# Performance work log

Hardware: AMD Instinct MI355X
Metric: run time of the kernel (lower is better)

Reference implementation:

```python
import jax, jax.numpy as jnp
import numpy as np

D_MODEL = 1024
NUM_HEADS = 16
D_K = D_MODEL // NUM_HEADS


def setup_inputs() -> dict:
    key = jax.random.key(0)
    ks = jax.random.split(key, 11)
    s = 1.0 / np.sqrt(D_MODEL)
    inp = {
        "Q": jax.random.normal(ks[0], (2, 2048, D_MODEL), jnp.float32),
        "K": jax.random.normal(ks[1], (2, 2048, D_MODEL), jnp.float32),
        "V": jax.random.normal(ks[2], (2, 2048, D_MODEL), jnp.float32),
        "W_q": jax.random.uniform(ks[3], (D_MODEL, D_MODEL), jnp.float32, -s, s),
        "b_q": jax.random.uniform(ks[4], (D_MODEL,), jnp.float32, -s, s),
        "W_k": jax.random.uniform(ks[5], (D_MODEL, D_MODEL), jnp.float32, -s, s),
        "b_k": jax.random.uniform(ks[6], (D_MODEL,), jnp.float32, -s, s),
        "W_v": jax.random.uniform(ks[7], (D_MODEL, D_MODEL), jnp.float32, -s, s),
        "b_v": jax.random.uniform(ks[8], (D_MODEL,), jnp.float32, -s, s),
        "W_o": jax.random.uniform(ks[9], (D_MODEL, D_MODEL), jnp.float32, -s, s),
        "b_o": jax.random.uniform(ks[10], (D_MODEL,), jnp.float32, -s, s),
    }
    return inp


def reference(Q, K, V, W_q, b_q, W_k, b_k, W_v, b_v, W_o, b_o):
    B, S, _ = Q.shape
    # Linear projections (torch Linear: x @ W.T + b; W here stored as [in, out])
    q = Q @ W_q + b_q
    k = K @ W_k + b_k
    v = V @ W_v + b_v
    # split heads -> [B, H, S, d_k]
    q = q.reshape(B, S, NUM_HEADS, D_K).transpose(0, 2, 1, 3)
    k = k.reshape(B, S, NUM_HEADS, D_K).transpose(0, 2, 1, 3)
    v = v.reshape(B, S, NUM_HEADS, D_K).transpose(0, 2, 1, 3)
    scale = 1.0 / np.sqrt(D_K).astype(np.float32)
    scores = jnp.einsum('bhqd,bhkd->bhqk', q, k) * scale  # [B,H,S,S]
    probs = jax.nn.softmax(scores, axis=-1)
    attn = jnp.einsum('bhqk,bhkd->bhqd', probs, v)  # [B,H,S,d_k]
    attn = attn.transpose(0, 2, 1, 3).reshape(B, S, D_MODEL)
    return attn @ W_o + b_o
```

## Files before the change

kernel.cpp:

```cpp
#include <hip/hip_runtime.h>
#include <math.h>

#define SEQ   2048
#define DM    1024
#define NH    16
#define DK    64
#define MTOT  4096
#define QSCALE 0.18033688011112043f

typedef __bf16 bf16x8 __attribute__((ext_vector_type(8)));
typedef float  f32x4  __attribute__((ext_vector_type(4)));
typedef unsigned short u16;
typedef unsigned long long u64;

__device__ __forceinline__ u16 f2bf(float f) {
    unsigned int u = __float_as_uint(f);
    u += 0x7fff + ((u >> 16) & 1);
    return (u16)(u >> 16);
}

__device__ __forceinline__ void async16(const void* g, void* l) {
    __builtin_amdgcn_global_load_lds(
        (const __attribute__((address_space(1))) unsigned int*)(unsigned long long)g,
        (__attribute__((address_space(3))) unsigned int*)(unsigned int)(unsigned long long)l,
        16, 0, 0);
}

__device__ __forceinline__ bf16x8 ld16(const u16* p) {
    bf16x8 v;
    __builtin_memcpy(&v, p, 16);
    return v;
}
__device__ __forceinline__ bf16x8 ld8x2(const u16* p) {
    union { u64 q[2]; bf16x8 v; } u;
    __builtin_memcpy(&u.q[0], p, 8);
    __builtin_memcpy(&u.q[1], p + 4, 8);
    return u.v;
}
__device__ __forceinline__ void st8(u16* p, unsigned int lo, unsigned int hi) {
    u64 q = ((u64)hi << 32) | lo;
    __builtin_memcpy(p, &q, 8);
}

__global__ __launch_bounds__(256)
void cvt_in(const float* __restrict__ Q, const float* __restrict__ K,
            const float* __restrict__ V, u16* __restrict__ Qb,
            u16* __restrict__ Kb, u16* __restrict__ Vb)
{
    const float* src; u16* dst;
    if (blockIdx.z == 0)      { src = Q; dst = Qb; }
    else if (blockIdx.z == 1) { src = K; dst = Kb; }
    else                      { src = V; dst = Vb; }
    const size_t i = ((size_t)blockIdx.x * 256 + threadIdx.x) * 8;
    float4 a = *(const float4*)&src[i];
    float4 b = *(const float4*)&src[i + 4];
    uint4 o;
    o.x = (unsigned)f2bf(a.x) | ((unsigned)f2bf(a.y) << 16);
    o.y = (unsigned)f2bf(a.z) | ((unsigned)f2bf(a.w) << 16);
    o.z = (unsigned)f2bf(b.x) | ((unsigned)f2bf(b.y) << 16);
    o.w = (unsigned)f2bf(b.z) | ((unsigned)f2bf(b.w) << 16);
    *(uint4*)&dst[i] = o;
}

__global__ __launch_bounds__(256)
void cvt_wt(const float* __restrict__ Wq, const float* __restrict__ Wk,
            const float* __restrict__ Wv, const float* __restrict__ Wo,
            u16* __restrict__ Tq, u16* __restrict__ Tk,
            u16* __restrict__ Tv, u16* __restrict__ To)
{
    const float* W; u16* Wt;
    if (blockIdx.z == 0)      { W = Wq; Wt = Tq; }
    else if (blockIdx.z == 1) { W = Wk; Wt = Tk; }
    else if (blockIdx.z == 2) { W = Wv; Wt = Tv; }
    else                      { W = Wo; Wt = To; }
    __shared__ float Ts[64][65];
    const int t = threadIdx.x;
    const int k0 = blockIdx.x * 64, n0 = blockIdx.y * 64;
#pragma unroll
    for (int p = 0; p < 4; ++p) {
        const int flat = t + p * 256;
        const int r = flat >> 4, c4 = (flat & 15) * 4;
        float4 v = *(const float4*)&W[(size_t)(k0 + r) * DM + n0 + c4];
        Ts[r][c4 + 0] = v.x; Ts[r][c4 + 1] = v.y;
        Ts[r][c4 + 2] = v.z; Ts[r][c4 + 3] = v.w;
    }
    __syncthreads();
#pragma unroll
    for (int p = 0; p < 2; ++p) {
        const int flat = t + p * 256;
        const int n = flat >> 3, kc = (flat & 7) * 8;
        uint4 o;
        o.x = (unsigned)f2bf(Ts[kc + 0][n]) | ((unsigned)f2bf(Ts[kc + 1][n]) << 16);
        o.y = (unsigned)f2bf(Ts[kc + 2][n]) | ((unsigned)f2bf(Ts[kc + 3][n]) << 16);
        o.z = (unsigned)f2bf(Ts[kc + 4][n]) | ((unsigned)f2bf(Ts[kc + 5][n]) << 16);
        o.w = (unsigned)f2bf(Ts[kc + 6][n]) | ((unsigned)f2bf(Ts[kc + 7][n]) << 16);
        *(uint4*)&Wt[(size_t)(n0 + n) * DM + k0 + kc] = o;
    }
}

template <int SCATTER>
__device__ __forceinline__ void gemm_core(const u16* __restrict__ A,
                                          const u16* __restrict__ Wt,
                                          const float* __restrict__ bias,
                                          void* __restrict__ Out, float scale)
{
    __shared__ u16 As[128 * 32];
    __shared__ u16 Bs[128 * 32];

    const int tid = threadIdx.x;
    const int lane = tid & 63;
    const int wv = __builtin_amdgcn_readfirstlane(tid >> 6);
    const int wm = wv >> 1, wn = wv & 1;
    const int lane15 = lane & 15, quad = lane >> 4;
    const int row0 = blockIdx.x * 128, col0 = blockIdx.y * 128;

    const int arow = lane >> 2;
    const int acol = (lane & 3) * 8;

    f32x4 acc[4][4];
#pragma unroll
    for (int i = 0; i < 4; ++i)
#pragma unroll
        for (int j = 0; j < 4; ++j) acc[i][j] = (f32x4)0.f;

    for (int k0 = 0; k0 < DM; k0 += 32) {
#pragma unroll
        for (int cc = 0; cc < 2; ++cc) {
            const int c = 2 * wv + cc;
            async16(&A[(size_t)(row0 + c * 16 + arow) * DM + k0 + acol],
                    &As[c * 512]);
            async16(&Wt[(size_t)(col0 + c * 16 + arow) * DM + k0 + acol],
                    &Bs[c * 512]);
        }
        __syncthreads();

        bf16x8 af[4];
#pragma unroll
        for (int mi = 0; mi < 4; ++mi)
            af[mi] = ld16(&As[(wm * 64 + mi * 16 + lane15) * 32 + quad * 8]);
#pragma unroll
        for (int ni = 0; ni < 4; ++ni) {
            bf16x8 bfrag = ld16(&Bs[(wn * 64 + ni * 16 + lane15) * 32 + quad * 8]);
#pragma unroll
            for (int mi = 0; mi < 4; ++mi)
                acc[mi][ni] = __builtin_amdgcn_mfma_f32_16x16x32_bf16(
                    af[mi], bfrag, acc[mi][ni], 0, 0, 0);
        }
        __syncthreads();
    }

#pragma unroll
    for (int mi = 0; mi < 4; ++mi) {
        const int mbase = row0 + wm * 64 + mi * 16 + quad * 4;
#pragma unroll
        for (int ni = 0; ni < 4; ++ni) {
            const int n = col0 + wn * 64 + ni * 16 + lane15;
            const float bz = bias[n];
            if (SCATTER == 1) {
                const int h = n >> 6, dk = n & 63;
#pragma unroll
                for (int r = 0; r < 4; ++r) {
                    const int mm = mbase + r;
                    const int b_ = mm >> 11, s = mm & 2047;
                    ((u16*)Out)[(((size_t)(b_ * NH + h)) * SEQ + s) * DK + dk] =
                        f2bf((acc[mi][ni][r] + bz) * scale);
                }
            } else if (SCATTER == 2) {
                const int h = n >> 6, dk = n & 63;
                const int b_ = mbase >> 11, s0 = mbase & 2047;
                u64 q = (u64)f2bf((acc[mi][ni][0] + bz) * scale)
                      | ((u64)f2bf((acc[mi][ni][1] + bz) * scale) << 16)
                      | ((u64)f2bf((acc[mi][ni][2] + bz) * scale) << 32)
                      | ((u64)f2bf((acc[mi][ni][3] + bz) * scale) << 48);
                u16* dst = (u16*)Out +
                    (((size_t)(b_ * NH + h)) * DK + dk) * SEQ + s0;
                __builtin_memcpy(dst, &q, 8);
            } else {
#pragma unroll
                for (int r = 0; r < 4; ++r) {
                    const int mm = mbase + r;
                    ((float*)Out)[(size_t)mm * DM + n] = acc[mi][ni][r] + bz;
                }
            }
        }
    }
}

__global__ __launch_bounds__(256)
void qkv_gemm(const u16* __restrict__ Qb, const u16* __restrict__ Kb,
              const u16* __restrict__ Vb,
              const u16* __restrict__ Tq, const u16* __restrict__ Tk,
              const u16* __restrict__ Tv,
              const float* __restrict__ bq, const float* __restrict__ bk,
              const float* __restrict__ bv,
              u16* __restrict__ qw, u16* __restrict__ kw, u16* __restrict__ vtw)
{
    if (blockIdx.z == 0)      gemm_core<1>(Qb, Tq, bq, qw, QSCALE);
    else if (blockIdx.z == 1) gemm_core<1>(Kb, Tk, bk, kw, 1.0f);
    else                      gemm_core<2>(Vb, Tv, bv, vtw, 1.0f);
}

__global__ __launch_bounds__(256)
void out_gemm(const u16* __restrict__ A, const u16* __restrict__ Wt,
              const float* __restrict__ bias, float* __restrict__ Out)
{
    __shared__ u16 As[128 * 32];
    __shared__ u16 Bs[64 * 32];

    const int tid = threadIdx.x;
    const int lane = tid & 63;
    const int wv = __builtin_amdgcn_readfirstlane(tid >> 6);
    const int wm = wv >> 1, wn = wv & 1;
    const int lane15 = lane & 15, quad = lane >> 4;
    const int row0 = blockIdx.x * 128, col0 = blockIdx.y * 64;

    const int arow = lane >> 2;
    const int acol = (lane & 3) * 8;

    f32x4 acc[4][2];
#pragma unroll
    for (int i = 0; i < 4; ++i)
#pragma unroll
        for (int j = 0; j < 2; ++j) acc[i][j] = (f32x4)0.f;

    for (int k0 = 0; k0 < DM; k0 += 32) {
#pragma unroll
        for (int cc = 0; cc < 2; ++cc) {
            const int c = 2 * wv + cc;
            async16(&A[(size_t)(row0 + c * 16 + arow) * DM + k0 + acol],
                    &As[c * 512]);
        }
        async16(&Wt[(size_t)(col0 + wv * 16 + arow) * DM + k0 + acol],
                &Bs[wv * 512]);
        __syncthreads();

        bf16x8 af[4];
#pragma unroll
        for (int mi = 0; mi < 4; ++mi)
            af[mi] = ld16(&As[(wm * 64 + mi * 16 + lane15) * 32 + quad * 8]);
#pragma unroll
        for (int ni = 0; ni < 2; ++ni) {
            bf16x8 bfrag = ld16(&Bs[(wn * 32 + ni * 16 + lane15) * 32 + quad * 8]);
#pragma unroll
            for (int mi = 0; mi < 4; ++mi)
                acc[mi][ni] = __builtin_amdgcn_mfma_f32_16x16x32_bf16(
                    af[mi], bfrag, acc[mi][ni], 0, 0, 0);
        }
        __syncthreads();
    }

#pragma unroll
    for (int mi = 0; mi < 4; ++mi) {
        const int mbase = row0 + wm * 64 + mi * 16 + quad * 4;
#pragma unroll
        for (int ni = 0; ni < 2; ++ni) {
            const int n = col0 + wn * 32 + ni * 16 + lane15;
            const float bz = bias[n];
#pragma unroll
            for (int r = 0; r < 4; ++r)
                Out[(size_t)(mbase + r) * DM + n] = acc[mi][ni][r] + bz;
        }
    }
}

__global__ __launch_bounds__(256)
void attn_mfma(const u16* __restrict__ qw, const u16* __restrict__ kw,
               const u16* __restrict__ vt, u16* __restrict__ attnb)
{
    __shared__ u16 Qs[128 * 68];
    __shared__ u16 Ks[64 * 68];
    __shared__ u16 Vts[64 * 68];
    __shared__ u16 Ps[4][32 * 68];

    const int tid = threadIdx.x;
    const int lane = tid & 63;
    const int wv = tid >> 6;
    const int lane15 = lane & 15, quad = lane >> 4;
    const int bh = blockIdx.x;
    const int q0 = blockIdx.y * 128;
    const size_t base = (size_t)bh * SEQ * DK;

    const int lr = tid >> 3;
    const int lc = (tid & 7) * 8;

#pragma unroll
    for (int i = 0; i < 4; ++i) {
        const int flat = tid + i * 256;
        const int r = flat >> 3, c = (flat & 7) * 8;
        uint4 v = *(const uint4*)&qw[base + (size_t)(q0 + r) * DK + c];
        st8(&Qs[r * 68 + c], v.x, v.y);
        st8(&Qs[r * 68 + c + 4], v.z, v.w);
    }
    __syncthreads();

    bf16x8 qa[2][2];
#pragma unroll
    for (int mi = 0; mi < 2; ++mi)
#pragma unroll
        for (int kk = 0; kk < 2; ++kk)
            qa[mi][kk] = ld8x2(&Qs[(wv * 32 + mi * 16 + lane15) * 68 +
                                   kk * 32 + quad * 8]);

    u16* Pw = &Ps[wv][0];

    f32x4 o_acc[2][4];
    float lpart[8];
#pragma unroll
    for (int mi = 0; mi < 2; ++mi)
#pragma unroll
        for (int nd = 0; nd < 4; ++nd) o_acc[mi][nd] = (f32x4)0.f;
#pragma unroll
    for (int r = 0; r < 8; ++r) lpart[r] = 0.f;

#pragma unroll
    for (int i = 0; i < 2; ++i) {
        const int r = lr + i * 32, c = lc;
        uint4 kv = *(const uint4*)&kw[base + (size_t)r * DK + c];
        st8(&Ks[r * 68 + c], kv.x, kv.y);
        st8(&Ks[r * 68 + c + 4], kv.z, kv.w);
        uint4 vv = *(const uint4*)&vt[base + (size_t)r * SEQ + c];
        st8(&Vts[r * 68 + c], vv.x, vv.y);
        st8(&Vts[r * 68 + c + 4], vv.z, vv.w);
    }
    __syncthreads();

    for (int c0 = 0; c0 < SEQ; c0 += 64) {
        uint4 kpre[2], vpre[2];
        const bool more = (c0 + 64 < SEQ);
        if (more) {
#pragma unroll
            for (int i = 0; i < 2; ++i) {
                const int r = lr + i * 32;
                kpre[i] = *(const uint4*)&kw[base + (size_t)(c0 + 64 + r) * DK + lc];
                vpre[i] = *(const uint4*)&vt[base + (size_t)r * SEQ + c0 + 64 + lc];
            }
        }

        f32x4 s_acc[2][4];
#pragma unroll
        for (int mi = 0; mi < 2; ++mi)
#pragma unroll
            for (int ni = 0; ni < 4; ++ni) s_acc[mi][ni] = (f32x4)0.f;
#pragma unroll
        for (int ni = 0; ni < 4; ++ni)
#pragma unroll
            for (int kk = 0; kk < 2; ++kk) {
                bf16x8 kb = ld8x2(&Ks[(ni * 16 + lane15) * 68 + kk * 32 + quad * 8]);
#pragma unroll
                for (int mi = 0; mi < 2; ++mi)
                    s_acc[mi][ni] = __builtin_amdgcn_mfma_f32_16x16x32_bf16(
                        qa[mi][kk], kb, s_acc[mi][ni], 0, 0, 0);
            }

#pragma unroll
        for (int mi = 0; mi < 2; ++mi)
#pragma unroll
            for (int ni = 0; ni < 4; ++ni)
#pragma unroll
                for (int r = 0; r < 4; ++r) {
                    const float p = exp2f(s_acc[mi][ni][r]);
                    lpart[mi * 4 + r] += p;
                    Pw[(mi * 16 + quad * 4 + r) * 68 + ni * 16 + lane15] = f2bf(p);
                }

        bf16x8 pa[2][2];
#pragma unroll
        for (int mi = 0; mi < 2; ++mi)
#pragma unroll
            for (int kk = 0; kk < 2; ++kk)
                pa[mi][kk] = ld8x2(&Pw[(mi * 16 + lane15) * 68 + kk * 32 + quad * 8]);
#pragma unroll
        for (int nd = 0; nd < 4; ++nd)
#pragma unroll
            for (int kk = 0; kk < 2; ++kk) {
                bf16x8 vb = ld8x2(&Vts[(nd * 16 + lane15) * 68 + kk * 32 + quad * 8]);
#pragma unroll
                for (int mi = 0; mi < 2; ++mi)
                    o_acc[mi][nd] = __builtin_amdgcn_mfma_f32_16x16x32_bf16(
                        pa[mi][kk], vb, o_acc[mi][nd], 0, 0, 0);
            }
        __syncthreads();

        if (more) {
#pragma unroll
            for (int i = 0; i < 2; ++i) {
                const int r = lr + i * 32, c = lc;
                st8(&Ks[r * 68 + c], kpre[i].x, kpre[i].y);
                st8(&Ks[r * 68 + c + 4], kpre[i].z, kpre[i].w);
                st8(&Vts[r * 68 + c], vpre[i].x, vpre[i].y);
                st8(&Vts[r * 68 + c + 4], vpre[i].z, vpre[i].w);
            }
        }
        __syncthreads();
    }

#pragma unroll
    for (int idx = 0; idx < 8; ++idx) {
        float l = lpart[idx];
        l += __shfl_xor(l, 1);
        l += __shfl_xor(l, 2);
        l += __shfl_xor(l, 4);
        l += __shfl_xor(l, 8);
        lpart[idx] = 1.f / l;
    }

    const int b_ = bh >> 4, h = bh & 15;
#pragma unroll
    for (int mi = 0; mi < 2; ++mi)
#pragma unroll
        for (int r = 0; r < 4; ++r) {
            const int srow = q0 + wv * 32 + mi * 16 + quad * 4 + r;
            const float inv = lpart[mi * 4 + r];
#pragma unroll
            for (int nd = 0; nd < 4; ++nd)
                attnb[((size_t)b_ * SEQ + srow) * DM + h * DK + nd * 16 + lane15] =
                    f2bf(o_acc[mi][nd][r] * inv);
        }
}

extern "C" void kernel_launch(void* const* d_in, const int* in_sizes, int n_in,
                              void* d_out, int out_size, void* d_ws, size_t ws_size,
                              hipStream_t stream)
{
    const float* Q  = (const float*)d_in[0];
    const float* K  = (const float*)d_in[1];
    const float* V  = (const float*)d_in[2];
    const float* Wq = (const float*)d_in[3];
    const float* bq = (const float*)d_in[4];
    const float* Wk = (const float*)d_in[5];
    const float* bk = (const float*)d_in[6];
    const float* Wv = (const float*)d_in[7];
    const float* bv = (const float*)d_in[8];
    const float* Wo = (const float*)d_in[9];
    const float* bo = (const float*)d_in[10];
    float* out = (float*)d_out;

    const size_t MB = 1024 * 1024;
    char* w8 = (char*)d_ws;
    u16* Qbf = (u16*)(w8 + 0 * MB);
    u16* Kbf = (u16*)(w8 + 8 * MB);
    u16* Vbf = (u16*)(w8 + 16 * MB);
    u16* Wtq = (u16*)(w8 + 24 * MB);
    u16* Wtk = (u16*)(w8 + 26 * MB);
    u16* Wtv = (u16*)(w8 + 28 * MB);
    u16* Wto = (u16*)(w8 + 30 * MB);
    u16* qw  = (u16*)(w8 + 32 * MB);
    u16* kw  = (u16*)(w8 + 40 * MB);
    u16* vtw = (u16*)(w8 + 48 * MB);
    u16* attnb = Qbf;

    cvt_in<<<dim3(2048, 1, 3), 256, 0, stream>>>(Q, K, V, Qbf, Kbf, Vbf);
    cvt_wt<<<dim3(16, 16, 4), 256, 0, stream>>>(Wq, Wk, Wv, Wo,
                                                Wtq, Wtk, Wtv, Wto);
    qkv_gemm<<<dim3(32, 8, 3), 256, 0, stream>>>(Qbf, Kbf, Vbf, Wtq, Wtk, Wtv,
                                                 bq, bk, bv, qw, kw, vtw);
    attn_mfma<<<dim3(32, 16), 256, 0, stream>>>(qw, kw, vtw, attnb);
    out_gemm<<<dim3(32, 16), 256, 0, stream>>>(attnb, Wto, bo, out);
}
```

Before: 244.2 us.

## Widen GEMM K-tiles, halve attention query tile, permute P/V layout

Both projection GEMMs now stage 64-wide K slices in LDS per iteration instead of 32, which halves the number of barrier-separated loop trips. The attention kernel drops from 128 to 64 query rows per block, doubling the grid and cutting per-wave registers and LDS. It also writes P with packed bf16 perm stores and permutes V^T columns in LDS so the layouts match. Exp uses the raw hardware intrinsic and bf16 packing switches to round-half-up, which may shift numerics slightly and doubles K/V reloads per query row.

```diff
diff --git a/kernel.cpp b/kernel.cpp
--- a/kernel.cpp
+++ b/kernel.cpp
@@ -104,8 +104,8 @@
                                           const float* __restrict__ bias,
                                           void* __restrict__ Out, float scale)
 {
-    __shared__ u16 As[128 * 32];
-    __shared__ u16 Bs[128 * 32];
+    __shared__ u16 As[128 * 64];
+    __shared__ u16 Bs[128 * 64];
 
     const int tid = threadIdx.x;
     const int lane = tid & 63;
@@ -114,8 +114,8 @@
     const int lane15 = lane & 15, quad = lane >> 4;
     const int row0 = blockIdx.x * 128, col0 = blockIdx.y * 128;
 
-    const int arow = lane >> 2;
-    const int acol = (lane & 3) * 8;
+    const int arow = lane >> 3;
+    const int acol = (lane & 7) * 8;
 
     f32x4 acc[4][4];
 #pragma unroll
@@ -123,28 +123,33 @@
 #pragma unroll
         for (int j = 0; j < 4; ++j) acc[i][j] = (f32x4)0.f;
 
-    for (int k0 = 0; k0 < DM; k0 += 32) {
-#pragma unroll
-        for (int cc = 0; cc < 2; ++cc) {
-            const int c = 2 * wv + cc;
-            async16(&A[(size_t)(row0 + c * 16 + arow) * DM + k0 + acol],
+    for (int k0 = 0; k0 < DM; k0 += 64) {
+#pragma unroll
+        for (int cc = 0; cc < 4; ++cc) {
+            const int c = 4 * wv + cc;
+            async16(&A[(size_t)(row0 + c * 8 + arow) * DM + k0 + acol],
                     &As[c * 512]);
-            async16(&Wt[(size_t)(col0 + c * 16 + arow) * DM + k0 + acol],
+            async16(&Wt[(size_t)(col0 + c * 8 + arow) * DM + k0 + acol],
                     &Bs[c * 512]);
         }
         __syncthreads();
 
-        bf16x8 af[4];
-#pragma unroll
-        for (int mi = 0; mi < 4; ++mi)
-            af[mi] = ld16(&As[(wm * 64 + mi * 16 + lane15) * 32 + quad * 8]);
-#pragma unroll
-        for (int ni = 0; ni < 4; ++ni) {
-            bf16x8 bfrag = ld16(&Bs[(wn * 64 + ni * 16 + lane15) * 32 + quad * 8]);
+#pragma unroll
+        for (int kk = 0; kk < 2; ++kk) {
+            bf16x8 af[4];
 #pragma unroll
             for (int mi = 0; mi < 4; ++mi)
-                acc[mi][ni] = __builtin_amdgcn_mfma_f32_16x16x32_bf16(
-                    af[mi], bfrag, acc[mi][ni], 0, 0, 0);
+                af[mi] = ld16(&As[(wm * 64 + mi * 16 + lane15) * 64 +
+                                  kk * 32 + quad * 8]);
+#pragma unroll
+            for (int ni = 0; ni < 4; ++ni) {
+                bf16x8 bfrag = ld16(&Bs[(wn * 64 + ni * 16 + lane15) * 64 +
+                                        kk * 32 + quad * 8]);
+#pragma unroll
+                for (int mi = 0; mi < 4; ++mi)
+                    acc[mi][ni] = __builtin_amdgcn_mfma_f32_16x16x32_bf16(
+                        af[mi], bfrag, acc[mi][ni], 0, 0, 0);
+            }
         }
         __syncthreads();
     }
@@ -204,8 +209,8 @@
 void out_gemm(const u16* __restrict__ A, const u16* __restrict__ Wt,
               const float* __restrict__ bias, float* __restrict__ Out)
 {
-    __shared__ u16 As[128 * 32];
-    __shared__ u16 Bs[64 * 32];
+    __shared__ u16 As[128 * 64];
+    __shared__ u16 Bs[64 * 64];
 
     const int tid = threadIdx.x;
     const int lane = tid & 63;
@@ -214,8 +219,8 @@
     const int lane15 = lane & 15, quad = lane >> 4;
     const int row0 = blockIdx.x * 128, col0 = blockIdx.y * 64;
 
-    const int arow = lane >> 2;
-    const int acol = (lane & 3) * 8;
+    const int arow = lane >> 3;
+    const int acol = (lane & 7) * 8;
 
     f32x4 acc[4][2];
 #pragma unroll
@@ -223,28 +228,37 @@
 #pragma unroll
         for (int j = 0; j < 2; ++j) acc[i][j] = (f32x4)0.f;
 
-    for (int k0 = 0; k0 < DM; k0 += 32) {
+    for (int k0 = 0; k0 < DM; k0 += 64) {
+#pragma unroll
+        for (int cc = 0; cc < 4; ++cc) {
+            const int c = 4 * wv + cc;
+            async16(&A[(size_t)(row0 + c * 8 + arow) * DM + k0 + acol],
+                    &As[c * 512]);
+        }
 #pragma unroll
         for (int cc = 0; cc < 2; ++cc) {
             const int c = 2 * wv + cc;
-            async16(&A[(size_t)(row0 + c * 16 + arow) * DM + k0 + acol],
-                    &As[c * 512]);
-        }
-        async16(&Wt[(size_t)(col0 + wv * 16 + arow) * DM + k0 + acol],
-                &Bs[wv * 512]);
-        __syncthreads();
-
-        bf16x8 af[4];
-#pragma unroll
-        for (int mi = 0; mi < 4; ++mi)
-            af[mi] = ld16(&As[(wm * 64 + mi * 16 + lane15) * 32 + quad * 8]);
-#pragma unroll
-        for (int ni = 0; ni < 2; ++ni) {
-            bf16x8 bfrag = ld16(&Bs[(wn * 32 + ni * 16 + lane15) * 32 + quad * 8]);
+            async16(&Wt[(size_t)(col0 + c * 8 + arow) * DM + k0 + acol],
+                    &Bs[c * 512]);
+        }
+        __syncthreads();
+
+#pragma unroll
+        for (int kk = 0; kk < 2; ++kk) {
+            bf16x8 af[4];
 #pragma unroll
             for (int mi = 0; mi < 4; ++mi)
-                acc[mi][ni] = __builtin_amdgcn_mfma_f32_16x16x32_bf16(
-                    af[mi], bfrag, acc[mi][ni], 0, 0, 0);
+                af[mi] = ld16(&As[(wm * 64 + mi * 16 + lane15) * 64 +
+                                  kk * 32 + quad * 8]);
+#pragma unroll
+            for (int ni = 0; ni < 2; ++ni) {
+                bf16x8 bfrag = ld16(&Bs[(wn * 32 + ni * 16 + lane15) * 64 +
+                                        kk * 32 + quad * 8]);
+#pragma unroll
+                for (int mi = 0; mi < 4; ++mi)
+                    acc[mi][ni] = __builtin_amdgcn_mfma_f32_16x16x32_bf16(
+                        af[mi], bfrag, acc[mi][ni], 0, 0, 0);
+            }
         }
         __syncthreads();
     }
@@ -267,24 +281,25 @@
 void attn_mfma(const u16* __restrict__ qw, const u16* __restrict__ kw,
                const u16* __restrict__ vt, u16* __restrict__ attnb)
 {
-    __shared__ u16 Qs[128 * 68];
+    __shared__ u16 Qs[64 * 68];
     __shared__ u16 Ks[64 * 68];
     __shared__ u16 Vts[64 * 68];
-    __shared__ u16 Ps[4][32 * 68];
+    __shared__ u16 Ps[4][16 * 68];
 
     const int tid = threadIdx.x;
     const int lane = tid & 63;
     const int wv = tid >> 6;
     const int lane15 = lane & 15, quad = lane >> 4;
     const int bh = blockIdx.x;
-    const int q0 = blockIdx.y * 128;
+    const int q0 = blockIdx.y * 64;
     const size_t base = (size_t)bh * SEQ * DK;
 
     const int lr = tid >> 3;
     const int lc = (tid & 7) * 8;
-
-#pragma unroll
-    for (int i = 0; i < 4; ++i) {
+    const int vbase = (lc & 15) * 4 + (lc >> 4);
+
+#pragma unroll
+    for (int i = 0; i < 2; ++i) {
         const int flat = tid + i * 256;
         const int r = flat >> 3, c = (flat & 7) * 8;
         uint4 v = *(const uint4*)&qw[base + (size_t)(q0 + r) * DK + c];
@@ -293,34 +308,31 @@
     }
     __syncthreads();
 
-    bf16x8 qa[2][2];
-#pragma unroll
-    for (int mi = 0; mi < 2; ++mi)
-#pragma unroll
-        for (int kk = 0; kk < 2; ++kk)
-            qa[mi][kk] = ld8x2(&Qs[(wv * 32 + mi * 16 + lane15) * 68 +
-                                   kk * 32 + quad * 8]);
+    bf16x8 qa[2];
+#pragma unroll
+    for (int kk = 0; kk < 2; ++kk)
+        qa[kk] = ld8x2(&Qs[(wv * 16 + lane15) * 68 + kk * 32 + quad * 8]);
 
     u16* Pw = &Ps[wv][0];
 
-    f32x4 o_acc[2][4];
-    float lpart[8];
-#pragma unroll
-    for (int mi = 0; mi < 2; ++mi)
-#pragma unroll
-        for (int nd = 0; nd < 4; ++nd) o_acc[mi][nd] = (f32x4)0.f;
-#pragma unroll
-    for (int r = 0; r < 8; ++r) lpart[r] = 0.f;
+    f32x4 o_acc[4];
+    float lpart[4];
+#pragma unroll
+    for (int nd = 0; nd < 4; ++nd) o_acc[nd] = (f32x4)0.f;
+#pragma unroll
+    for (int r = 0; r < 4; ++r) lpart[r] = 0.f;
 
 #pragma unroll
     for (int i = 0; i < 2; ++i) {
-        const int r = lr + i * 32, c = lc;
-        uint4 kv = *(const uint4*)&kw[base + (size_t)r * DK + c];
-        st8(&Ks[r * 68 + c], kv.x, kv.y);
-        st8(&Ks[r * 68 + c + 4], kv.z, kv.w);
-        uint4 vv = *(const uint4*)&vt[base + (size_t)r * SEQ + c];
-        st8(&Vts[r * 68 + c], vv.x, vv.y);
-        st8(&Vts[r * 68 + c + 4], vv.z, vv.w);
+        const int r = lr + i * 32;
+        uint4 kv = *(const uint4*)&kw[base + (size_t)r * DK + lc];
+        st8(&Ks[r * 68 + lc], kv.x, kv.y);
+        st8(&Ks[r * 68 + lc + 4], kv.z, kv.w);
+        union { uint4 u; u16 s[8]; } vu;
+        vu.u = *(const uint4*)&vt[base + (size_t)r * SEQ + lc];
+#pragma unroll
+        for (int j = 0; j < 8; ++j)
+            Vts[r * 68 + vbase + 4 * j] = vu.s[j];
     }
     __syncthreads();
 
@@ -336,86 +348,82 @@
             }
         }
 
-        f32x4 s_acc[2][4];
-#pragma unroll
-        for (int mi = 0; mi < 2; ++mi)
-#pragma unroll
-            for (int ni = 0; ni < 4; ++ni) s_acc[mi][ni] = (f32x4)0.f;
+        f32x4 s_acc[4];
+#pragma unroll
+        for (int ni = 0; ni < 4; ++ni) s_acc[ni] = (f32x4)0.f;
 #pragma unroll
         for (int ni = 0; ni < 4; ++ni)
 #pragma unroll
             for (int kk = 0; kk < 2; ++kk) {
                 bf16x8 kb = ld8x2(&Ks[(ni * 16 + lane15) * 68 + kk * 32 + quad * 8]);
-#pragma unroll
-                for (int mi = 0; mi < 2; ++mi)
-                    s_acc[mi][ni] = __builtin_amdgcn_mfma_f32_16x16x32_bf16(
-                        qa[mi][kk], kb, s_acc[mi][ni], 0, 0, 0);
-            }
-
-#pragma unroll
-        for (int mi = 0; mi < 2; ++mi)
-#pragma unroll
-            for (int ni = 0; ni < 4; ++ni)
-#pragma unroll
-                for (int r = 0; r < 4; ++r) {
-                    const float p = exp2f(s_acc[mi][ni][r]);
-                    lpart[mi * 4 + r] += p;
-                    Pw[(mi * 16 + quad * 4 + r) * 68 + ni * 16 + lane15] = f2bf(p);
-                }
-
-        bf16x8 pa[2][2];
-#pragma unroll
-        for (int mi = 0; mi < 2; ++mi)
-#pragma unroll
-            for (int kk = 0; kk < 2; ++kk)
-                pa[mi][kk] = ld8x2(&Pw[(mi * 16 + lane15) * 68 + kk * 32 + quad * 8]);
+                s_acc[ni] = __builtin_amdgcn_mfma_f32_16x16x32_bf16(
+                    qa[kk], kb, s_acc[ni], 0, 0, 0);
+            }
+
+#pragma unroll
+        for (int r = 0; r < 4; ++r) {
+            unsigned int u[4];
+#pragma unroll
+            for (int ni = 0; ni < 4; ++ni) {
+                const float p = __builtin_amdgcn_exp2f(s_acc[ni][r]);
+                lpart[r] += p;
+                u[ni] = __float_as_uint(p) + 0x8000u;
+            }
+            const unsigned int lo = __builtin_amdgcn_perm(u[1], u[0], 0x07060302u);
+            const unsigned int hi = __builtin_amdgcn_perm(u[3], u[2], 0x07060302u);
+            st8(&Pw[(quad * 4 + r) * 68 + lane15 * 4], lo, hi);
+        }
+
+        bf16x8 pa[2];
+#pragma unroll
+        for (int kk = 0; kk < 2; ++kk)
+            pa[kk] = ld8x2(&Pw[lane15 * 68 + kk * 32 + quad * 8]);
 #pragma unroll
         for (int nd = 0; nd < 4; ++nd)
 #pragma unroll
             for (int kk = 0; kk < 2; ++kk) {
                 bf16x8 vb = ld8x2(&Vts[(nd * 16 + lane15) * 68 + kk * 32 + quad * 8]);
-#pragma unroll
-                for (int mi = 0; mi < 2; ++mi)
-                    o_acc[mi][nd] = __builtin_amdgcn_mfma_f32_16x16x32_bf16(
-                        pa[mi][kk], vb, o_acc[mi][nd], 0, 0, 0);
+                o_acc[nd] = __builtin_amdgcn_mfma_f32_16x16x32_bf16(
+                    pa[kk], vb, o_acc[nd], 0, 0, 0);
             }
         __syncthreads();
 
         if (more) {
 #pragma unroll
             for (int i = 0; i < 2; ++i) {
-                const int r = lr + i * 32, c = lc;
-                st8(&Ks[r * 68 + c], kpre[i].x, kpre[i].y);
-                st8(&Ks[r * 68 + c + 4], kpre[i].z, kpre[i].w);
-                st8(&Vts[r * 68 + c], vpre[i].x, vpre[i].y);
-                st8(&Vts[r * 68 + c + 4], vpre[i].z, vpre[i].w);
-            }
-        }
-        __syncthreads();
-    }
-
-#pragma unroll
-    for (int idx = 0; idx < 8; ++idx) {
-        float l = lpart[idx];
+                const int r = lr + i * 32;
+                st8(&Ks[r * 68 + lc], kpre[i].x, kpre[i].y);
+                st8(&Ks[r * 68 + lc + 4], kpre[i].z, kpre[i].w);
+                union { uint4 u; u16 s[8]; } vu;
+                vu.u = vpre[i];
+#pragma unroll
+                for (int j = 0; j < 8; ++j)
+                    Vts[r * 68 + vbase + 4 * j] = vu.s[j];
+            }
+        }
+        __syncthreads();
+    }
+
+#pragma unroll
+    for (int r = 0; r < 4; ++r) {
+        float l = lpart[r];
         l += __shfl_xor(l, 1);
         l += __shfl_xor(l, 2);
         l += __shfl_xor(l, 4);
         l += __shfl_xor(l, 8);
-        lpart[idx] = 1.f / l;
+        lpart[r] = 1.f / l;
     }
 
     const int b_ = bh >> 4, h = bh & 15;
 #pragma unroll
-    for (int mi = 0; mi < 2; ++mi)
-#pragma unroll
-        for (int r = 0; r < 4; ++r) {
-            const int srow = q0 + wv * 32 + mi * 16 + quad * 4 + r;
-            const float inv = lpart[mi * 4 + r];
-#pragma unroll
-            for (int nd = 0; nd < 4; ++nd)
-                attnb[((size_t)b_ * SEQ + srow) * DM + h * DK + nd * 16 + lane15] =
-                    f2bf(o_acc[mi][nd][r] * inv);
-        }
+    for (int r = 0; r < 4; ++r) {
+        const int srow = q0 + wv * 16 + quad * 4 + r;
+        const float inv = lpart[r];
+#pragma unroll
+        for (int nd = 0; nd < 4; ++nd)
+            attnb[((size_t)b_ * SEQ + srow) * DM + h * DK + nd * 16 + lane15] =
+                f2bf(o_acc[nd][r] * inv);
+    }
 }
 
 extern "C" void kernel_launch(void* const* d_in, const int* in_sizes, int n_in,
@@ -454,6 +462,6 @@
                                                 Wtq, Wtk, Wtv, Wto);
     qkv_gemm<<<dim3(32, 8, 3), 256, 0, stream>>>(Qbf, Kbf, Vbf, Wtq, Wtk, Wtv,
                                                  bq, bk, bv, qw, kw, vtw);
-    attn_mfma<<<dim3(32, 16), 256, 0, stream>>>(qw, kw, vtw, attnb);
+    attn_mfma<<<dim3(32, 32), 256, 0, stream>>>(qw, kw, vtw, attnb);
     out_gemm<<<dim3(32, 16), 256, 0, stream>>>(attnb, Wto, bo, out);
 }
```

After: 261.4 us. 7.0% more time.

## Split attention over keys, add combine pass, deepen GEMM K-step

Applied to the files above, without the earlier changes.

The attention kernel is restructured into 2048 blocks of 128 threads. Each block handles 64 queries and half of the key range, using an XCD-aware block-to-head mapping. Partial unnormalized outputs and row sums go to workspace, and a new combine kernel merges and normalizes them. This raises occupancy and parallelism at the cost of an extra pass and bf16 rounding of the partials. The change also packs P stores through perm, stores V transposed in LDS to allow vectorized P writes, and doubles the K-step per barrier in both GEMMs so each sync covers more MFMA work.

```diff
diff --git a/kernel.cpp b/kernel.cpp
--- a/kernel.cpp
+++ b/kernel.cpp
@@ -104,8 +104,8 @@
                                           const float* __restrict__ bias,
                                           void* __restrict__ Out, float scale)
 {
-    __shared__ u16 As[128 * 32];
-    __shared__ u16 Bs[128 * 32];
+    __shared__ u16 As[2][128 * 32];
+    __shared__ u16 Bs[2][128 * 32];
 
     const int tid = threadIdx.x;
     const int lane = tid & 63;
@@ -123,28 +123,34 @@
 #pragma unroll
         for (int j = 0; j < 4; ++j) acc[i][j] = (f32x4)0.f;
 
-    for (int k0 = 0; k0 < DM; k0 += 32) {
-#pragma unroll
-        for (int cc = 0; cc < 2; ++cc) {
-            const int c = 2 * wv + cc;
-            async16(&A[(size_t)(row0 + c * 16 + arow) * DM + k0 + acol],
-                    &As[c * 512]);
-            async16(&Wt[(size_t)(col0 + c * 16 + arow) * DM + k0 + acol],
-                    &Bs[c * 512]);
+    for (int k0 = 0; k0 < DM; k0 += 64) {
+#pragma unroll
+        for (int p = 0; p < 2; ++p) {
+#pragma unroll
+            for (int cc = 0; cc < 2; ++cc) {
+                const int c = 2 * wv + cc;
+                async16(&A[(size_t)(row0 + c * 16 + arow) * DM + k0 + p * 32 + acol],
+                        &As[p][c * 512]);
+                async16(&Wt[(size_t)(col0 + c * 16 + arow) * DM + k0 + p * 32 + acol],
+                        &Bs[p][c * 512]);
+            }
         }
         __syncthreads();
 
-        bf16x8 af[4];
-#pragma unroll
-        for (int mi = 0; mi < 4; ++mi)
-            af[mi] = ld16(&As[(wm * 64 + mi * 16 + lane15) * 32 + quad * 8]);
-#pragma unroll
-        for (int ni = 0; ni < 4; ++ni) {
-            bf16x8 bfrag = ld16(&Bs[(wn * 64 + ni * 16 + lane15) * 32 + quad * 8]);
+#pragma unroll
+        for (int kk = 0; kk < 2; ++kk) {
+            bf16x8 af[4];
 #pragma unroll
             for (int mi = 0; mi < 4; ++mi)
-                acc[mi][ni] = __builtin_amdgcn_mfma_f32_16x16x32_bf16(
-                    af[mi], bfrag, acc[mi][ni], 0, 0, 0);
+                af[mi] = ld16(&As[kk][(wm * 64 + mi * 16 + lane15) * 32 + quad * 8]);
+#pragma unroll
+            for (int ni = 0; ni < 4; ++ni) {
+                bf16x8 bfrag = ld16(&Bs[kk][(wn * 64 + ni * 16 + lane15) * 32 + quad * 8]);
+#pragma unroll
+                for (int mi = 0; mi < 4; ++mi)
+                    acc[mi][ni] = __builtin_amdgcn_mfma_f32_16x16x32_bf16(
+                        af[mi], bfrag, acc[mi][ni], 0, 0, 0);
+            }
         }
         __syncthreads();
     }
@@ -204,8 +210,8 @@
 void out_gemm(const u16* __restrict__ A, const u16* __restrict__ Wt,
               const float* __restrict__ bias, float* __restrict__ Out)
 {
-    __shared__ u16 As[128 * 32];
-    __shared__ u16 Bs[64 * 32];
+    __shared__ u16 As[2][128 * 32];
+    __shared__ u16 Bs[2][64 * 32];
 
     const int tid = threadIdx.x;
     const int lane = tid & 63;
@@ -223,28 +229,34 @@
 #pragma unroll
         for (int j = 0; j < 2; ++j) acc[i][j] = (f32x4)0.f;
 
-    for (int k0 = 0; k0 < DM; k0 += 32) {
-#pragma unroll
-        for (int cc = 0; cc < 2; ++cc) {
-            const int c = 2 * wv + cc;
-            async16(&A[(size_t)(row0 + c * 16 + arow) * DM + k0 + acol],
-                    &As[c * 512]);
-        }
-        async16(&Wt[(size_t)(col0 + wv * 16 + arow) * DM + k0 + acol],
-                &Bs[wv * 512]);
+    for (int k0 = 0; k0 < DM; k0 += 64) {
+#pragma unroll
+        for (int p = 0; p < 2; ++p) {
+#pragma unroll
+            for (int cc = 0; cc < 2; ++cc) {
+                const int c = 2 * wv + cc;
+                async16(&A[(size_t)(row0 + c * 16 + arow) * DM + k0 + p * 32 + acol],
+                        &As[p][c * 512]);
+            }
+            async16(&Wt[(size_t)(col0 + wv * 16 + arow) * DM + k0 + p * 32 + acol],
+                    &Bs[p][wv * 512]);
+        }
         __syncthreads();
 
-        bf16x8 af[4];
-#pragma unroll
-        for (int mi = 0; mi < 4; ++mi)
-            af[mi] = ld16(&As[(wm * 64 + mi * 16 + lane15) * 32 + quad * 8]);
-#pragma unroll
-        for (int ni = 0; ni < 2; ++ni) {
-            bf16x8 bfrag = ld16(&Bs[(wn * 32 + ni * 16 + lane15) * 32 + quad * 8]);
+#pragma unroll
+        for (int kk = 0; kk < 2; ++kk) {
+            bf16x8 af[4];
 #pragma unroll
             for (int mi = 0; mi < 4; ++mi)
-                acc[mi][ni] = __builtin_amdgcn_mfma_f32_16x16x32_bf16(
-                    af[mi], bfrag, acc[mi][ni], 0, 0, 0);
+                af[mi] = ld16(&As[kk][(wm * 64 + mi * 16 + lane15) * 32 + quad * 8]);
+#pragma unroll
+            for (int ni = 0; ni < 2; ++ni) {
+                bf16x8 bfrag = ld16(&Bs[kk][(wn * 32 + ni * 16 + lane15) * 32 + quad * 8]);
+#pragma unroll
+                for (int mi = 0; mi < 4; ++mi)
+                    acc[mi][ni] = __builtin_amdgcn_mfma_f32_16x16x32_bf16(
+                        af[mi], bfrag, acc[mi][ni], 0, 0, 0);
+            }
         }
         __syncthreads();
     }
@@ -263,43 +275,37 @@
     }
 }
 
-__global__ __launch_bounds__(256)
+__global__ __launch_bounds__(128, 3)
 void attn_mfma(const u16* __restrict__ qw, const u16* __restrict__ kw,
-               const u16* __restrict__ vt, u16* __restrict__ attnb)
-{
-    __shared__ u16 Qs[128 * 68];
+               const u16* __restrict__ vt, u16* __restrict__ opart,
+               float* __restrict__ lw)
+{
     __shared__ u16 Ks[64 * 68];
     __shared__ u16 Vts[64 * 68];
-    __shared__ u16 Ps[4][32 * 68];
+    __shared__ u16 Ps[2][32 * 68];
 
     const int tid = threadIdx.x;
     const int lane = tid & 63;
     const int wv = tid >> 6;
     const int lane15 = lane & 15, quad = lane >> 4;
-    const int bh = blockIdx.x;
-    const int q0 = blockIdx.y * 128;
+
+    const int flat = blockIdx.x;
+    const int xcd = flat & 7;
+    const int rest = flat >> 3;
+    const int bh = xcd * 4 + (rest & 3);
+    const int qt = (rest >> 2) & 31;
+    const int ks = rest >> 7;
+    const int q0 = qt * 64;
+    const int c0beg = ks * 1024;
     const size_t base = (size_t)bh * SEQ * DK;
 
-    const int lr = tid >> 3;
-    const int lc = (tid & 7) * 8;
-
-#pragma unroll
-    for (int i = 0; i < 4; ++i) {
-        const int flat = tid + i * 256;
-        const int r = flat >> 3, c = (flat & 7) * 8;
-        uint4 v = *(const uint4*)&qw[base + (size_t)(q0 + r) * DK + c];
-        st8(&Qs[r * 68 + c], v.x, v.y);
-        st8(&Qs[r * 68 + c + 4], v.z, v.w);
-    }
-    __syncthreads();
-
     bf16x8 qa[2][2];
 #pragma unroll
     for (int mi = 0; mi < 2; ++mi)
 #pragma unroll
         for (int kk = 0; kk < 2; ++kk)
-            qa[mi][kk] = ld8x2(&Qs[(wv * 32 + mi * 16 + lane15) * 68 +
-                                   kk * 32 + quad * 8]);
+            qa[mi][kk] = ld16(&qw[base +
+                (size_t)(q0 + wv * 32 + mi * 16 + lane15) * DK + kk * 32 + quad * 8]);
 
     u16* Pw = &Ps[wv][0];
 
@@ -312,27 +318,33 @@
 #pragma unroll
     for (int r = 0; r < 8; ++r) lpart[r] = 0.f;
 
-#pragma unroll
-    for (int i = 0; i < 2; ++i) {
-        const int r = lr + i * 32, c = lc;
-        uint4 kv = *(const uint4*)&kw[base + (size_t)r * DK + c];
-        st8(&Ks[r * 68 + c], kv.x, kv.y);
-        st8(&Ks[r * 68 + c + 4], kv.z, kv.w);
-        uint4 vv = *(const uint4*)&vt[base + (size_t)r * SEQ + c];
-        st8(&Vts[r * 68 + c], vv.x, vv.y);
-        st8(&Vts[r * 68 + c + 4], vv.z, vv.w);
+    const int sr = tid >> 1;
+    const int sh = (tid & 1) * 32;
+
+#pragma unroll
+    for (int j = 0; j < 4; ++j) {
+        const int c = sh + j * 8;
+        const int cb = (c & 15) * 4 + (c >> 4);
+        uint4 kv = *(const uint4*)&kw[base + (size_t)(c0beg + sr) * DK + c];
+        st8(&Ks[sr * 68 + c], kv.x, kv.y);
+        st8(&Ks[sr * 68 + c + 4], kv.z, kv.w);
+        union { uint4 u; u16 s[8]; } vu;
+        vu.u = *(const uint4*)&vt[base + (size_t)sr * SEQ + c0beg + c];
+#pragma unroll
+        for (int e = 0; e < 8; ++e) Vts[sr * 68 + cb + 4 * e] = vu.s[e];
     }
     __syncthreads();
 
-    for (int c0 = 0; c0 < SEQ; c0 += 64) {
-        uint4 kpre[2], vpre[2];
-        const bool more = (c0 + 64 < SEQ);
+    for (int it = 0; it < 16; ++it) {
+        const int c0 = c0beg + it * 64;
+        uint4 kpre[4], vpre[4];
+        const bool more = (it < 15);
         if (more) {
 #pragma unroll
-            for (int i = 0; i < 2; ++i) {
-                const int r = lr + i * 32;
-                kpre[i] = *(const uint4*)&kw[base + (size_t)(c0 + 64 + r) * DK + lc];
-                vpre[i] = *(const uint4*)&vt[base + (size_t)r * SEQ + c0 + 64 + lc];
+            for (int j = 0; j < 4; ++j) {
+                const int c = sh + j * 8;
+                kpre[j] = *(const uint4*)&kw[base + (size_t)(c0 + 64 + sr) * DK + c];
+                vpre[j] = *(const uint4*)&vt[base + (size_t)sr * SEQ + c0 + 64 + c];
             }
         }
 
@@ -355,13 +367,18 @@
 #pragma unroll
         for (int mi = 0; mi < 2; ++mi)
 #pragma unroll
-            for (int ni = 0; ni < 4; ++ni)
-#pragma unroll
-                for (int r = 0; r < 4; ++r) {
-                    const float p = exp2f(s_acc[mi][ni][r]);
+            for (int r = 0; r < 4; ++r) {
+                unsigned int u[4];
+#pragma unroll
+                for (int ni = 0; ni < 4; ++ni) {
+                    const float p = __builtin_amdgcn_exp2f(s_acc[mi][ni][r]);
                     lpart[mi * 4 + r] += p;
-                    Pw[(mi * 16 + quad * 4 + r) * 68 + ni * 16 + lane15] = f2bf(p);
+                    u[ni] = __float_as_uint(p) + 0x8000u;
                 }
+                const unsigned int lo = __builtin_amdgcn_perm(u[1], u[0], 0x07060302u);
+                const unsigned int hi = __builtin_amdgcn_perm(u[3], u[2], 0x07060302u);
+                st8(&Pw[(mi * 16 + quad * 4 + r) * 68 + lane15 * 4], lo, hi);
+            }
 
         bf16x8 pa[2][2];
 #pragma unroll
@@ -383,39 +400,66 @@
 
         if (more) {
 #pragma unroll
-            for (int i = 0; i < 2; ++i) {
-                const int r = lr + i * 32, c = lc;
-                st8(&Ks[r * 68 + c], kpre[i].x, kpre[i].y);
-                st8(&Ks[r * 68 + c + 4], kpre[i].z, kpre[i].w);
-                st8(&Vts[r * 68 + c], vpre[i].x, vpre[i].y);
-                st8(&Vts[r * 68 + c + 4], vpre[i].z, vpre[i].w);
+            for (int j = 0; j < 4; ++j) {
+                const int c = sh + j * 8;
+                const int cb = (c & 15) * 4 + (c >> 4);
+                st8(&Ks[sr * 68 + c], kpre[j].x, kpre[j].y);
+                st8(&Ks[sr * 68 + c + 4], kpre[j].z, kpre[j].w);
+                union { uint4 u; u16 s[8]; } vu;
+                vu.u = vpre[j];
+#pragma unroll
+                for (int e = 0; e < 8; ++e) Vts[sr * 68 + cb + 4 * e] = vu.s[e];
             }
         }
         __syncthreads();
     }
 
-#pragma unroll
-    for (int idx = 0; idx < 8; ++idx) {
-        float l = lpart[idx];
-        l += __shfl_xor(l, 1);
-        l += __shfl_xor(l, 2);
-        l += __shfl_xor(l, 4);
-        l += __shfl_xor(l, 8);
-        lpart[idx] = 1.f / l;
-    }
-
+    const size_t obase = ((size_t)(ks * 32 + bh)) * SEQ;
+#pragma unroll
+    for (int mi = 0; mi < 2; ++mi)
+#pragma unroll
+        for (int r = 0; r < 4; ++r) {
+            const int s = q0 + wv * 32 + mi * 16 + quad * 4 + r;
+            float l = lpart[mi * 4 + r];
+            l += __shfl_xor(l, 1);
+            l += __shfl_xor(l, 2);
+            l += __shfl_xor(l, 4);
+            l += __shfl_xor(l, 8);
+            if (lane15 == 0)
+                lw[(size_t)(ks * 32 + bh) * SEQ + s] = l;
+#pragma unroll
+            for (int nd = 0; nd < 4; ++nd)
+                opart[(obase + s) * DK + nd * 16 + lane15] = f2bf(o_acc[mi][nd][r]);
+        }
+}
+
+__global__ __launch_bounds__(256)
+void attn_combine(const u16* __restrict__ opart, const float* __restrict__ lw,
+                  u16* __restrict__ attnb)
+{
+    const int flat = blockIdx.x * 256 + threadIdx.x;
+    const int dv = (flat & 7) * 8;
+    const int s  = (flat >> 3) & 2047;
+    const int bh = flat >> 14;
+    const size_t i0 = ((size_t)bh * SEQ + s) * DK + dv;
+    const size_t i1 = i0 + (size_t)32 * SEQ * DK;
+    uint4 a = *(const uint4*)&opart[i0];
+    uint4 b = *(const uint4*)&opart[i1];
+    const float l = lw[(size_t)bh * SEQ + s] + lw[(size_t)(32 + bh) * SEQ + s];
+    const float inv = 1.f / l;
+    unsigned int au[4] = {a.x, a.y, a.z, a.w};
+    unsigned int bu[4] = {b.x, b.y, b.z, b.w};
+    unsigned int ou[4];
+#pragma unroll
+    for (int j = 0; j < 4; ++j) {
+        const float e0 = __uint_as_float(au[j] << 16) + __uint_as_float(bu[j] << 16);
+        const float e1 = __uint_as_float(au[j] & 0xffff0000u) +
+                         __uint_as_float(bu[j] & 0xffff0000u);
+        ou[j] = (unsigned)f2bf(e0 * inv) | ((unsigned)f2bf(e1 * inv) << 16);
+    }
     const int b_ = bh >> 4, h = bh & 15;
-#pragma unroll
-    for (int mi = 0; mi < 2; ++mi)
-#pragma unroll
-        for (int r = 0; r < 4; ++r) {
-            const int srow = q0 + wv * 32 + mi * 16 + quad * 4 + r;
-            const float inv = lpart[mi * 4 + r];
-#pragma unroll
-            for (int nd = 0; nd < 4; ++nd)
-                attnb[((size_t)b_ * SEQ + srow) * DM + h * DK + nd * 16 + lane15] =
-                    f2bf(o_acc[mi][nd][r] * inv);
-        }
+    uint4 o; o.x = ou[0]; o.y = ou[1]; o.z = ou[2]; o.w = ou[3];
+    *(uint4*)&attnb[((size_t)b_ * SEQ + s) * DM + h * DK + dv] = o;
 }
 
 extern "C" void kernel_launch(void* const* d_in, const int* in_sizes, int n_in,
@@ -447,6 +491,8 @@
     u16* qw  = (u16*)(w8 + 32 * MB);
     u16* kw  = (u16*)(w8 + 40 * MB);
     u16* vtw = (u16*)(w8 + 48 * MB);
+    u16* opart = Kbf;
+    float* lwb = (float*)(w8 + 56 * MB);
     u16* attnb = Qbf;
 
     cvt_in<<<dim3(2048, 1, 3), 256, 0, stream>>>(Q, K, V, Qbf, Kbf, Vbf);
@@ -454,6 +500,7 @@
                                                 Wtq, Wtk, Wtv, Wto);
     qkv_gemm<<<dim3(32, 8, 3), 256, 0, stream>>>(Qbf, Kbf, Vbf, Wtq, Wtk, Wtv,
                                                  bq, bk, bv, qw, kw, vtw);
-    attn_mfma<<<dim3(32, 16), 256, 0, stream>>>(qw, kw, vtw, attnb);
+    attn_mfma<<<2048, 128, 0, stream>>>(qw, kw, vtw, opart, lwb);
+    attn_combine<<<2048, 256, 0, stream>>>(opart, lwb, attnb);
     out_gemm<<<dim3(32, 16), 256, 0, stream>>>(attnb, Wto, bo, out);
 }
```

New measurement: 249.9 us. +2.3%, slower.
